# Optimization experiments

Hardware: AMD Instinct MI355X
Metric: run time of the kernel (lower is better)

The kernel has to match this reference:

```python
import jax, jax.numpy as jnp
import numpy as np

B, T, TR, D, H = 8, 1024, 256, 1024, 16
HS = D // H  # head size = 64
FF = 4 * D


def _ln(x, g, b, eps=1e-5):
    m = jnp.mean(x, axis=-1, keepdims=True)
    v = jnp.mean((x - m) ** 2, axis=-1, keepdims=True)
    return (x - m) * jax.lax.rsqrt(v + eps) * g + b


def setup_inputs() -> dict:
    key = jax.random.key(0)
    ks = jax.random.split(key, 24)
    w = lambda i, shape: jax.random.normal(ks[i], shape, dtype=jnp.float32) * 0.02
    return {
        "x": jax.random.normal(ks[0], (B, T, D), dtype=jnp.float32),
        # reduced positional embedding table (gathered by arange == table itself)
        "pos_emb": w(1, (TR, D)),
        # inner standard Block params
        "blk_ln1_g": jnp.ones((D,), jnp.float32), "blk_ln1_b": jnp.zeros((D,), jnp.float32),
        "blk_wq": w(2, (H, D, HS)), "blk_wk": w(3, (H, D, HS)), "blk_wv": w(4, (H, D, HS)),
        "blk_wo": w(5, (D, D)), "blk_bo": jnp.zeros((D,), jnp.float32),
        "blk_ln2_g": jnp.ones((D,), jnp.float32), "blk_ln2_b": jnp.zeros((D,), jnp.float32),
        "blk_w1": w(6, (D, FF)), "blk_b1": jnp.zeros((FF,), jnp.float32),
        "blk_w2": w(7, (FF, D)), "blk_b2": jnp.zeros((D,), jnp.float32),
        # compressing cross-attention params
        "ln1_g": jnp.ones((D,), jnp.float32), "ln1_b": jnp.zeros((D,), jnp.float32),
        "ca_wq": w(8, (H, D, HS)), "ca_wk": w(9, (H, D, HS)), "ca_wv": w(10, (H, D, HS)),
        "ca_wo": w(11, (D, D)), "ca_bo": jnp.zeros((D,), jnp.float32),
        "ln2_g": jnp.ones((D,), jnp.float32), "ln2_b": jnp.zeros((D,), jnp.float32),
        "ff_w1": w(12, (D, FF)), "ff_b1": jnp.zeros((FF,), jnp.float32),
        "ff_w2": w(13, (FF, D)), "ff_b2": jnp.zeros((D,), jnp.float32),
    }


def reference(x, pos_emb, blk_ln1_g, blk_ln1_b, blk_wq, blk_wk, blk_wv, blk_wo, blk_bo,
              blk_ln2_g, blk_ln2_b, blk_w1, blk_b1, blk_w2, blk_b2,
              ln1_g, ln1_b, ca_wq, ca_wk, ca_wv, ca_wo, ca_bo,
              ln2_g, ln2_b, ff_w1, ff_b1, ff_w2, ff_b2):
    b, t, c = x.shape
    scale = c ** -0.5  # matches q @ k^T * c**-0.5 in source

    # ---- inner standard Block: y = x + sa(ln1(x)); y = y + ffwd(ln2(y)) ----
    h = _ln(x, blk_ln1_g, blk_ln1_b)
    q = jnp.einsum('btc,hcs->bhts', h, blk_wq)
    k = jnp.einsum('btc,hcs->bhts', h, blk_wk)
    v = jnp.einsum('btc,hcs->bhts', h, blk_wv)
    wei = jnp.einsum('bhts,bhus->bhtu', q, k) * scale
    causal = jnp.tril(jnp.ones((t, t), dtype=bool))
    wei = jax.nn.softmax(jnp.where(causal, wei, -jnp.inf), axis=-1)
    att = jnp.einsum('bhtu,bhus->bhts', wei, v)
    att = att.transpose(0, 2, 1, 3).reshape(b, t, c) @ blk_wo + blk_bo
    y = x + att
    h2 = _ln(y, blk_ln2_g, blk_ln2_b)
    y = y + (jax.nn.relu(h2 @ blk_w1 + blk_b1) @ blk_w2 + blk_b2)

    # outer residual in CompressingBlock.forward
    x = x + y

    # ---- compressing cross-attention: queries/values from x, keys from pos emb ----
    h1 = _ln(x, ln1_g, ln1_b)
    q = jnp.einsum('btc,hcs->bhts', h1, ca_wq)
    kk = jnp.einsum('rc,hcs->hrs', pos_emb, ca_wk)  # same for every batch
    v = jnp.einsum('btc,hcs->bhts', h1, ca_wv)
    wei = jnp.einsum('bhts,hrs->bhtr', q, kk) * scale  # [b,h,t,tr]
    tr = pos_emb.shape[0]
    mask = jnp.tril(jnp.ones((t, tr), dtype=bool))  # tril[:t,:tr]
    wei = jax.nn.softmax(jnp.where(mask, wei, -jnp.inf), axis=-1)
    # transpose then wei^T @ v -> compressed sequence length tr
    out = jnp.einsum('bhtr,bhts->bhrs', wei, v)
    out = out.transpose(0, 2, 1, 3).reshape(b, tr, c) @ ca_wo + ca_bo

    # ---- final FFN with residual ----
    h3 = _ln(out, ln2_g, ln2_b)
    out = out + (jax.nn.relu(h3 @ ff_w1 + ff_b1) @ ff_w2 + ff_b2)
    return out
```

## Files before the change

kernel.cpp:

```cpp
#include <hip/hip_runtime.h>
#include <stdint.h>

typedef unsigned short u16;
typedef __attribute__((ext_vector_type(8))) short short8;
typedef __attribute__((ext_vector_type(4))) float f32x4;

#define MFMA16(A,B,C) __builtin_amdgcn_mfma_f32_16x16x32_bf16(A,B,C,0,0,0)

static __device__ __forceinline__ u16 f2bf(float f) {
  union { float f; unsigned u; } v; v.f = f;
  unsigned r = v.u + 0x7FFFu + ((v.u >> 16) & 1u);
  return (u16)(r >> 16);
}

static __device__ __forceinline__ void gload16(const void* g, void* l) {
  __builtin_amdgcn_global_load_lds(
      (const __attribute__((address_space(1))) void*)(uintptr_t)g,
      (__attribute__((address_space(3))) void*)(uint32_t)(uintptr_t)l,
      16, 0, 0);
}

static __device__ __forceinline__ int xcd_swz() {
  const int gx = gridDim.x, gy = gridDim.y, nwg = gx * gy;
  const int orig = blockIdx.y * gx + blockIdx.x;
  const int q = nwg >> 3, rm = nwg & 7, xcd = orig & 7, idx = orig >> 3;
  return (xcd < rm ? xcd * (q + 1) : rm * (q + 1) + (xcd - rm) * q) + idx;
}

#define PHASEP(BUFO, KH, STAGE_STMT, TAIL_STMT) do { \
  short8 af_[4], bf_[4]; \
  _Pragma("unroll") \
  for (int mf = 0; mf < 4; ++mf) { \
    const int r = wm0 + mf * 16 + colL; \
    af_[mf] = *(const short8*)&lds[(BUFO) + ((KH) << 12) + r * 32 + ((kgr ^ ((r >> 1) & 3)) << 3)]; \
  } \
  _Pragma("unroll") \
  for (int nf = 0; nf < 4; ++nf) { \
    const int r = wn0 + nf * 16 + colL; \
    bf_[nf] = *(const short8*)&lds[(BUFO) + 8192 + ((KH) << 12) + r * 32 + ((kgr ^ ((r >> 1) & 3)) << 3)]; \
  } \
  STAGE_STMT; \
  __builtin_amdgcn_s_barrier(); \
  asm volatile("s_waitcnt lgkmcnt(0)" ::: "memory"); \
  __builtin_amdgcn_sched_barrier(0); \
  __builtin_amdgcn_s_setprio(1); \
  _Pragma("unroll") \
  for (int mf = 0; mf < 4; ++mf) \
    _Pragma("unroll") \
    for (int nf = 0; nf < 4; ++nf) \
      acc[mf][nf] = MFMA16(af_[mf], bf_[nf], acc[mf][nf]); \
  __builtin_amdgcn_s_setprio(0); \
  __builtin_amdgcn_sched_barrier(0); \
  TAIL_STMT; \
  __builtin_amdgcn_s_barrier(); \
} while (0)

__global__ __launch_bounds__(256) void gemm128p(
    const u16* __restrict__ A, const u16* __restrict__ Wt,
    float* __restrict__ Cf, u16* __restrict__ Cb,
    const float* __restrict__ bias,
    const float* __restrict__ res1, const float* __restrict__ res2,
    int M, int N, int K, int relu)
{
  __shared__ u16 lds[32768];
  const int tid = threadIdx.x;
  const int wid = tid >> 6, lane = tid & 63;
  const int colL = lane & 15, kgr = lane >> 4;
  const int wm0 = (wid & 1) * 64, wn0 = (wid >> 1) * 64;
  const int w = xcd_swz();
  const int m0 = (w / gridDim.y) * 128, n0 = (w % gridDim.y) * 128;
  const int NT = K >> 6;
  f32x4 acc[4][4] = {};

  auto stageP = [&](int t_, int kh) {
    const int kb = t_ * 64 + kh * 32;
    const int baseA = ((t_ & 1) << 14) + (kh << 12);
#pragma unroll
    for (int i = 0; i < 2; ++i) {
      const int c = i * 256 + tid;
      const int row = c >> 2, slot = c & 3;
      const int cs = kb + ((slot ^ ((row >> 1) & 3)) << 3);
      gload16(A  + (size_t)(m0 + row) * K + cs,
              &lds[baseA + ((i * 256 + wid * 64) << 3)]);
      gload16(Wt + (size_t)(n0 + row) * K + cs,
              &lds[baseA + 8192 + ((i * 256 + wid * 64) << 3)]);
    }
  };

  stageP(0, 0); stageP(0, 1); stageP(1, 0);
  asm volatile("s_waitcnt vmcnt(8)" ::: "memory");
  __builtin_amdgcn_s_barrier();

  for (int t = 0; t < NT; ++t) {
    const int bufo = (t & 1) << 14;
    PHASEP(bufo, 0,
           if (t + 1 < NT) stageP(t + 1, 1),
           if (t + 1 < NT) { asm volatile("s_waitcnt vmcnt(8)" ::: "memory"); }
           else            { asm volatile("s_waitcnt vmcnt(0)" ::: "memory"); } );
    PHASEP(bufo, 1,
           if (t + 2 < NT) stageP(t + 2, 0),
           if (t < NT - 2)       { asm volatile("s_waitcnt vmcnt(8)" ::: "memory"); }
           else if (t == NT - 2) { asm volatile("s_waitcnt vmcnt(4)" ::: "memory"); }
           else                  { asm volatile("s_waitcnt vmcnt(0)" ::: "memory"); } );
  }

#pragma unroll
  for (int mf = 0; mf < 4; ++mf) {
#pragma unroll
    for (int nf = 0; nf < 4; ++nf) {
      const int n = n0 + wn0 + nf * 16 + colL;
      const float bv = bias ? bias[n] : 0.f;
#pragma unroll
      for (int rr = 0; rr < 4; ++rr) {
        const int m = m0 + wm0 + mf * 16 + kgr * 4 + rr;
        const size_t off = (size_t)m * N + n;
        float v = acc[mf][nf][rr] + bv;
        if (res1) v += res1[off];
        if (res2) v += res2[off];
        if (relu) v = fmaxf(v, 0.f);
        if (Cf) Cf[off] = v; else Cb[off] = f2bf(v);
      }
    }
  }
}

__global__ __launch_bounds__(256) void ln_rows(
    const float* __restrict__ x, const float* __restrict__ g,
    const float* __restrict__ bt, u16* __restrict__ out)
{
  const int row = blockIdx.x, tid = threadIdx.x;
  const float4 v = ((const float4*)(x + (size_t)row * 1024))[tid];
  float s  = v.x + v.y + v.z + v.w;
  float ss = v.x * v.x + v.y * v.y + v.z * v.z + v.w * v.w;
#pragma unroll
  for (int off = 32; off; off >>= 1) {
    s  += __shfl_xor(s, off);
    ss += __shfl_xor(ss, off);
  }
  __shared__ float red[8];
  const int wid = tid >> 6, lane = tid & 63;
  if (lane == 0) { red[wid] = s; red[4 + wid] = ss; }
  __syncthreads();
  s  = red[0] + red[1] + red[2] + red[3];
  ss = red[4] + red[5] + red[6] + red[7];
  const float mean = s * 0.0009765625f;
  const float var  = ss * 0.0009765625f - mean * mean;
  const float rstd = rsqrtf(var + 1e-5f);
  const float4 gg = ((const float4*)g)[tid];
  const float4 bb = ((const float4*)bt)[tid];
  uint2 ov;
  ov.x = (unsigned)f2bf((v.x - mean) * rstd * gg.x + bb.x) |
         ((unsigned)f2bf((v.y - mean) * rstd * gg.y + bb.y) << 16);
  ov.y = (unsigned)f2bf((v.z - mean) * rstd * gg.z + bb.z) |
         ((unsigned)f2bf((v.w - mean) * rstd * gg.w + bb.w) << 16);
  *(uint2*)(out + (size_t)row * 1024 + tid * 4) = ov;
}

__global__ __launch_bounds__(256) void transpose_w(
    const float* __restrict__ in, u16* __restrict__ out, int R, int C)
{
  __shared__ float t[32][33];
  const int c0 = blockIdx.x * 32, r0 = blockIdx.y * 32;
  const int tx = threadIdx.x & 31, ty = threadIdx.x >> 5;
#pragma unroll
  for (int i = 0; i < 32; i += 8)
    t[ty + i][tx] = in[(size_t)(r0 + ty + i) * C + c0 + tx];
  __syncthreads();
#pragma unroll
  for (int i = 0; i < 32; i += 8)
    out[(size_t)(c0 + ty + i) * R + r0 + tx] = f2bf(t[tx][ty + i]);
}

__global__ __launch_bounds__(256) void pack_head_w(
    const float* __restrict__ w, u16* __restrict__ out)
{
  __shared__ float t[32][33];
  const int h = blockIdx.z;
  const int s0 = blockIdx.x * 32, c0 = blockIdx.y * 32;
  const int tx = threadIdx.x & 31, ty = threadIdx.x >> 5;
#pragma unroll
  for (int i = 0; i < 32; i += 8)
    t[ty + i][tx] = w[((size_t)h * 1024 + c0 + ty + i) * 64 + s0 + tx];
  __syncthreads();
#pragma unroll
  for (int i = 0; i < 32; i += 8)
    out[((size_t)h * 64 + s0 + ty + i) * 1024 + c0 + tx] = f2bf(t[tx][ty + i]);
}

__global__ __launch_bounds__(256) void cvt_bf16(
    const float* __restrict__ in, u16* __restrict__ out)
{
  const int i = blockIdx.x * blockDim.x + threadIdx.x;
  const float4 v = ((const float4*)in)[i];
  uint2 ov;
  ov.x = (unsigned)f2bf(v.x) | ((unsigned)f2bf(v.y) << 16);
  ov.y = (unsigned)f2bf(v.z) | ((unsigned)f2bf(v.w) << 16);
  *(uint2*)(out + (size_t)i * 4) = ov;
}

__global__ __launch_bounds__(256) void vtrans(
    const u16* __restrict__ src, u16* __restrict__ dst, int coloff, int ld)
{
  __shared__ u16 tile[64][65];
  const int t0 = blockIdx.x * 64, h = blockIdx.y, b = blockIdx.z;
  const int lr = threadIdx.x >> 4;
  const int lc = (threadIdx.x & 15) * 4;
#pragma unroll
  for (int i = 0; i < 64; i += 16) {
    const u16* sp = src + (size_t)(b * 1024 + t0 + lr + i) * ld + coloff + h * 64 + lc;
    const uint2 v = *(const uint2*)sp;
    tile[lr + i][lc + 0] = (u16)(v.x & 0xffff);
    tile[lr + i][lc + 1] = (u16)(v.x >> 16);
    tile[lr + i][lc + 2] = (u16)(v.y & 0xffff);
    tile[lr + i][lc + 3] = (u16)(v.y >> 16);
  }
  __syncthreads();
#pragma unroll
  for (int i = 0; i < 64; i += 16) {
    const int s = lr + i;
    uint2 ov;
    ov.x = (unsigned)tile[lc + 0][s] | ((unsigned)tile[lc + 1][s] << 16);
    ov.y = (unsigned)tile[lc + 2][s] | ((unsigned)tile[lc + 3][s] << 16);
    *(uint2*)(dst + (size_t)((b * 16 + h) * 64 + s) * 1024 + t0 + lc) = ov;
  }
}

__global__ __launch_bounds__(512) void attn_inner(
    const u16* __restrict__ qkv, const u16* __restrict__ vt,
    u16* __restrict__ att)
{
  __shared__ u16 Kl[128 * 64];
  __shared__ u16 Vl[64 * 128];
  __shared__ u16 Pl[8 * 16 * 128];
  const int tb = blockIdx.x, h = blockIdx.y, b = blockIdx.z;
  const int tid = threadIdx.x, wid = tid >> 6, lane = tid & 63;
  const int col = lane & 15, kgr = lane >> 4;
  const float scale = 0.03125f;
  short8 qf[2];
  {
    const int trow = tb * 128 + wid * 16 + col;
    const u16* qp = qkv + (size_t)(b * 1024 + trow) * 3072 + h * 64 + kgr * 8;
    qf[0] = *(const short8*)qp;
    qf[1] = *(const short8*)(qp + 32);
  }
  f32x4 o[4] = {};
  float mrun[4], lrun[4];
#pragma unroll
  for (int r = 0; r < 4; ++r) { mrun[r] = -1e30f; lrun[r] = 0.f; }

  for (int kt = 0; kt <= tb * 128; kt += 128) {
#pragma unroll
    for (int i = 0; i < 2; ++i) {
      const int e = i * 4096 + tid * 8;
      const int rk = e >> 6, uk = (e >> 3) & 7;
      gload16(qkv + (size_t)(b * 1024 + kt + rk) * 3072 + 1024 + h * 64 +
                  ((uk ^ (rk & 7)) << 3),
              &Kl[i * 4096 + wid * 512]);
      const int rv = e >> 7, uv = (e >> 3) & 15;
      gload16(vt + (size_t)((b * 16 + h) * 64 + rv) * 1024 + kt +
                  ((uv ^ (rv & 7)) << 3),
              &Vl[i * 4096 + wid * 512]);
    }
    __syncthreads();
    f32x4 s[8];
#pragma unroll
    for (int nt = 0; nt < 8; ++nt) {
      const int rk = nt * 16 + col;
      const short8 k0 = *(const short8*)&Kl[rk * 64 + ((kgr ^ (rk & 7)) << 3)];
      const short8 k1 = *(const short8*)&Kl[rk * 64 + (((kgr + 4) ^ (rk & 7)) << 3)];
      f32x4 a = {};
      a = MFMA16(qf[0], k0, a);
      a = MFMA16(qf[1], k1, a);
      s[nt] = a;
    }
    float mx[4];
#pragma unroll
    for (int r = 0; r < 4; ++r) mx[r] = -1e30f;
    const int tbase = tb * 128 + wid * 16 + kgr * 4;
    if (kt == tb * 128) {
#pragma unroll
      for (int nt = 0; nt < 8; ++nt) {
        const int kp = kt + nt * 16 + col;
#pragma unroll
        for (int r = 0; r < 4; ++r) {
          float v = s[nt][r] * scale;
          if (kp > tbase + r) v = -1e30f;
          s[nt][r] = v;
          mx[r] = fmaxf(mx[r], v);
        }
      }
    } else {
#pragma unroll
      for (int nt = 0; nt < 8; ++nt)
#pragma unroll
        for (int r = 0; r < 4; ++r) {
          const float v = s[nt][r] * scale;
          s[nt][r] = v;
          mx[r] = fmaxf(mx[r], v);
        }
    }
#pragma unroll
    for (int r = 0; r < 4; ++r)
#pragma unroll
      for (int off = 1; off < 16; off <<= 1)
        mx[r] = fmaxf(mx[r], __shfl_xor(mx[r], off));
    float f[4], rs[4];
#pragma unroll
    for (int r = 0; r < 4; ++r) {
      const float mn = fmaxf(mrun[r], mx[r]);
      f[r] = __expf(mrun[r] - mn);
      mrun[r] = mn;
      rs[r] = 0.f;
    }
#pragma unroll
    for (int nt = 0; nt < 8; ++nt)
#pragma unroll
      for (int r = 0; r < 4; ++r) {
        const float p = __expf(s[nt][r] - mrun[r]);
        s[nt][r] = p;
        rs[r] += p;
      }
#pragma unroll
    for (int r = 0; r < 4; ++r) {
#pragma unroll
      for (int off = 1; off < 16; off <<= 1)
        rs[r] += __shfl_xor(rs[r], off);
      lrun[r] = lrun[r] * f[r] + rs[r];
    }
#pragma unroll
    for (int st = 0; st < 4; ++st)
#pragma unroll
      for (int r = 0; r < 4; ++r)
        o[st][r] *= f[r];
    u16* pw = &Pl[wid * 2048];
#pragma unroll
    for (int nt = 0; nt < 8; ++nt)
#pragma unroll
      for (int r = 0; r < 4; ++r) {
        const int rp = kgr * 4 + r;
        pw[rp * 128 + ((nt * 16 + col) ^ ((rp & 7) << 3))] = f2bf(s[nt][r]);
      }
#pragma unroll
    for (int ks = 0; ks < 4; ++ks) {
      const short8 pa = *(const short8*)&pw[col * 128 +
          ((ks * 32 + kgr * 8) ^ ((col & 7) << 3))];
#pragma unroll
      for (int st = 0; st < 4; ++st) {
        const int rv = st * 16 + col;
        const short8 vb = *(const short8*)&Vl[rv * 128 +
            (((ks * 4 + kgr) ^ (rv & 7)) << 3)];
        o[st] = MFMA16(pa, vb, o[st]);
      }
    }
    __syncthreads();
  }
#pragma unroll
  for (int r = 0; r < 4; ++r) {
    const float inv = 1.f / lrun[r];
    const int t = tb * 128 + wid * 16 + kgr * 4 + r;
#pragma unroll
    for (int st = 0; st < 4; ++st)
      att[(size_t)(b * 1024 + t) * 1024 + h * 64 + st * 16 + col] =
          f2bf(o[st][r] * inv);
  }
}

__global__ __launch_bounds__(512) void attn_cross(
    const u16* __restrict__ qv, const u16* __restrict__ kk,
    const u16* __restrict__ vt, u16* __restrict__ outc)
{
  __shared__ u16 KKl[256 * 64];
  __shared__ u16 Vl[64 * 128];
  __shared__ u16 PTl[256 * 128];
  const int h = blockIdx.x, b = blockIdx.y;
  const int tid = threadIdx.x, wid = tid >> 6, lane = tid & 63;
  const int col = lane & 15, kgr = lane >> 4;
  const float scale = 0.03125f;
#pragma unroll
  for (int i = 0; i < 4; ++i) {
    const int e = i * 4096 + tid * 8;
    const int rk = e >> 6, uk = (e >> 3) & 7;
    gload16(kk + (size_t)rk * 1024 + h * 64 + ((uk ^ (rk & 7)) << 3),
            &KKl[i * 4096 + wid * 512]);
  }
  f32x4 oacc[2][4] = {};
  for (int tt = 0; tt < 8; ++tt) {
    const int t0 = tt * 128;
#pragma unroll
    for (int i = 0; i < 2; ++i) {
      const int e = i * 4096 + tid * 8;
      const int rv = e >> 7, uv = (e >> 3) & 15;
      gload16(vt + (size_t)((b * 16 + h) * 64 + rv) * 1024 + t0 +
                  ((uv ^ (rv & 7)) << 3),
              &Vl[i * 4096 + wid * 512]);
    }
    short8 qf0, qf1;
    {
      const int trow = t0 + wid * 16 + col;
      const u16* qp = qv + (size_t)(b * 1024 + trow) * 2048 + h * 64 + kgr * 8;
      qf0 = *(const short8*)qp;
      qf1 = *(const short8*)(qp + 32);
    }
    __syncthreads();
    f32x4 s[16];
#pragma unroll
    for (int rt = 0; rt < 16; ++rt) {
      const int rk = rt * 16 + col;
      const short8 k0 = *(const short8*)&KKl[rk * 64 + ((kgr ^ (rk & 7)) << 3)];
      const short8 k1 = *(const short8*)&KKl[rk * 64 + (((kgr + 4) ^ (rk & 7)) << 3)];
      f32x4 a = {};
      a = MFMA16(qf0, k0, a);
      a = MFMA16(qf1, k1, a);
      s[rt] = a;
    }
    float mx[4];
#pragma unroll
    for (int r = 0; r < 4; ++r) mx[r] = -1e30f;
    const int tbase = t0 + wid * 16 + kgr * 4;
    if (t0 < 256) {
#pragma unroll
      for (int rt = 0; rt < 16; ++rt) {
        const int rp = rt * 16 + col;
#pragma unroll
        for (int r = 0; r < 4; ++r) {
          float v = s[rt][r] * scale;
          if (rp > tbase + r) v = -1e30f;
          s[rt][r] = v;
          mx[r] = fmaxf(mx[r], v);
        }
      }
    } else {
#pragma unroll
      for (int rt = 0; rt < 16; ++rt)
#pragma unroll
        for (int r = 0; r < 4; ++r) {
          const float v = s[rt][r] * scale;
          s[rt][r] = v;
          mx[r] = fmaxf(mx[r], v);
        }
    }
#pragma unroll
    for (int r = 0; r < 4; ++r)
#pragma unroll
      for (int off = 1; off < 16; off <<= 1)
        mx[r] = fmaxf(mx[r], __shfl_xor(mx[r], off));
    float sm[4];
#pragma unroll
    for (int r = 0; r < 4; ++r) sm[r] = 0.f;
#pragma unroll
    for (int rt = 0; rt < 16; ++rt)
#pragma unroll
      for (int r = 0; r < 4; ++r) {
        const float p = __expf(s[rt][r] - mx[r]);
        s[rt][r] = p;
        sm[r] += p;
      }
#pragma unroll
    for (int r = 0; r < 4; ++r) {
#pragma unroll
      for (int off = 1; off < 16; off <<= 1)
        sm[r] += __shfl_xor(sm[r], off);
      sm[r] = 1.f / sm[r];
    }
#pragma unroll
    for (int rt = 0; rt < 16; ++rt)
#pragma unroll
      for (int r = 0; r < 4; ++r) {
        const int rpt = rt * 16 + col;
        PTl[rpt * 128 + ((wid * 16 + kgr * 4 + r) ^ ((rpt & 7) << 3))] =
            f2bf(s[rt][r] * sm[r]);
      }
    __syncthreads();
#pragma unroll
    for (int rr = 0; rr < 2; ++rr) {
      const int rb = (wid * 2 + rr) * 16;
#pragma unroll
      for (int ks = 0; ks < 4; ++ks) {
        const int rpt = rb + col;
        const short8 pa = *(const short8*)&PTl[rpt * 128 +
            ((ks * 32 + kgr * 8) ^ ((rpt & 7) << 3))];
#pragma unroll
        for (int st = 0; st < 4; ++st) {
          const int rv = st * 16 + col;
          const short8 vb = *(const short8*)&Vl[rv * 128 +
              (((ks * 4 + kgr) ^ (rv & 7)) << 3)];
          oacc[rr][st] = MFMA16(pa, vb, oacc[rr][st]);
        }
      }
    }
    __syncthreads();
  }
#pragma unroll
  for (int rr = 0; rr < 2; ++rr)
#pragma unroll
    for (int st = 0; st < 4; ++st)
#pragma unroll
      for (int r = 0; r < 4; ++r) {
        const int rpos = (wid * 2 + rr) * 16 + kgr * 4 + r;
        outc[(size_t)(b * 256 + rpos) * 1024 + h * 64 + st * 16 + col] =
            f2bf(oacc[rr][st][r]);
      }
}

extern "C" void kernel_launch(void* const* d_in, const int* in_sizes, int n_in,
                              void* d_out, int out_size, void* d_ws, size_t ws_size,
                              hipStream_t stream)
{
  const float* x     = (const float*)d_in[0];
  const float* pos   = (const float*)d_in[1];
  const float* bln1g = (const float*)d_in[2];
  const float* bln1b = (const float*)d_in[3];
  const float* bwq   = (const float*)d_in[4];
  const float* bwk   = (const float*)d_in[5];
  const float* bwv   = (const float*)d_in[6];
  const float* bwo   = (const float*)d_in[7];
  const float* bbo   = (const float*)d_in[8];
  const float* bln2g = (const float*)d_in[9];
  const float* bln2b = (const float*)d_in[10];
  const float* bw1   = (const float*)d_in[11];
  const float* bb1   = (const float*)d_in[12];
  const float* bw2   = (const float*)d_in[13];
  const float* bb2   = (const float*)d_in[14];
  const float* ln1g  = (const float*)d_in[15];
  const float* ln1b  = (const float*)d_in[16];
  const float* cwq   = (const float*)d_in[17];
  const float* cwk   = (const float*)d_in[18];
  const float* cwv   = (const float*)d_in[19];
  const float* cwo   = (const float*)d_in[20];
  const float* cbo   = (const float*)d_in[21];
  const float* cln2g = (const float*)d_in[22];
  const float* cln2b = (const float*)d_in[23];
  const float* fw1   = (const float*)d_in[24];
  const float* fb1   = (const float*)d_in[25];
  const float* fw2   = (const float*)d_in[26];
  const float* fb2   = (const float*)d_in[27];

  char* ws = (char*)d_ws;
  size_t off = 0;
  auto alloc = [&](size_t bytes) -> void* {
    void* p = ws + off; off += (bytes + 255) & ~(size_t)255; return p;
  };
  u16* wqkv_t = (u16*)alloc((size_t)3072 * 1024 * 2);
  u16* wo_t   = (u16*)alloc((size_t)1024 * 1024 * 2);
  u16* w1_t   = (u16*)alloc((size_t)4096 * 1024 * 2);
  u16* w2_t   = (u16*)alloc((size_t)1024 * 4096 * 2);
  u16* cwqv_t = (u16*)alloc((size_t)2048 * 1024 * 2);
  u16* cwk_t  = (u16*)alloc((size_t)1024 * 1024 * 2);
  u16* cwo_t  = (u16*)alloc((size_t)1024 * 1024 * 2);
  u16* fw1_t  = (u16*)alloc((size_t)4096 * 1024 * 2);
  u16* fw2_t  = (u16*)alloc((size_t)1024 * 4096 * 2);
  u16* pos_bf = (u16*)alloc((size_t)256 * 1024 * 2);
  u16* kkb    = (u16*)alloc((size_t)256 * 1024 * 2);
  u16* act_ln = (u16*)alloc((size_t)8192 * 1024 * 2);
  u16* qkv    = (u16*)alloc((size_t)8192 * 3072 * 2);
  u16* att    = (u16*)alloc((size_t)8192 * 1024 * 2);
  u16* ffb    = (u16*)alloc((size_t)8192 * 4096 * 2);
  float* yb   = (float*)alloc((size_t)8192 * 1024 * 4);
  if (ws_size < off) return;
  float* x2   = (float*)qkv;
  u16*   qv   = qkv;
  u16*   vt   = ffb;
  u16*   outc = att;
  float* zb   = yb;
  float* outp = (float*)d_out;

  const dim3 B256(256), B512(512);
  pack_head_w<<<dim3(2, 32, 16), B256, 0, stream>>>(bwq, wqkv_t);
  pack_head_w<<<dim3(2, 32, 16), B256, 0, stream>>>(bwk, wqkv_t + 1024 * 1024);
  pack_head_w<<<dim3(2, 32, 16), B256, 0, stream>>>(bwv, wqkv_t + 2048 * 1024);
  transpose_w<<<dim3(32, 32),  B256, 0, stream>>>(bwo, wo_t, 1024, 1024);
  transpose_w<<<dim3(128, 32), B256, 0, stream>>>(bw1, w1_t, 1024, 4096);
  transpose_w<<<dim3(32, 128), B256, 0, stream>>>(bw2, w2_t, 4096, 1024);
  pack_head_w<<<dim3(2, 32, 16), B256, 0, stream>>>(cwq, cwqv_t);
  pack_head_w<<<dim3(2, 32, 16), B256, 0, stream>>>(cwv, cwqv_t + 1024 * 1024);
  pack_head_w<<<dim3(2, 32, 16), B256, 0, stream>>>(cwk, cwk_t);
  transpose_w<<<dim3(32, 32),  B256, 0, stream>>>(cwo, cwo_t, 1024, 1024);
  transpose_w<<<dim3(128, 32), B256, 0, stream>>>(fw1, fw1_t, 1024, 4096);
  transpose_w<<<dim3(32, 128), B256, 0, stream>>>(fw2, fw2_t, 4096, 1024);
  cvt_bf16<<<dim3(256), B256, 0, stream>>>(pos, pos_bf);

  ln_rows<<<dim3(8192), B256, 0, stream>>>(x, bln1g, bln1b, act_ln);
  gemm128p<<<dim3(64, 24), B256, 0, stream>>>(act_ln, wqkv_t, nullptr, qkv,
      nullptr, nullptr, nullptr, 8192, 3072, 1024, 0);
  vtrans<<<dim3(16, 16, 8), B256, 0, stream>>>(qkv, vt, 2048, 3072);
  attn_inner<<<dim3(8, 16, 8), B512, 0, stream>>>(qkv, vt, att);
  gemm128p<<<dim3(64, 8), B256, 0, stream>>>(att, wo_t, yb, nullptr,
      bbo, x, nullptr, 8192, 1024, 1024, 0);
  ln_rows<<<dim3(8192), B256, 0, stream>>>(yb, bln2g, bln2b, act_ln);
  gemm128p<<<dim3(64, 32), B256, 0, stream>>>(act_ln, w1_t, nullptr, ffb,
      bb1, nullptr, nullptr, 8192, 4096, 1024, 1);
  gemm128p<<<dim3(64, 8), B256, 0, stream>>>(ffb, w2_t, x2, nullptr,
      bb2, yb, x, 8192, 1024, 4096, 0);

  ln_rows<<<dim3(8192), B256, 0, stream>>>(x2, ln1g, ln1b, act_ln);
  gemm128p<<<dim3(64, 16), B256, 0, stream>>>(act_ln, cwqv_t, nullptr, qv,
      nullptr, nullptr, nullptr, 8192, 2048, 1024, 0);
  gemm128p<<<dim3(2, 8), B256, 0, stream>>>(pos_bf, cwk_t, nullptr, kkb,
      nullptr, nullptr, nullptr, 256, 1024, 1024, 0);
  vtrans<<<dim3(16, 16, 8), B256, 0, stream>>>(qv, vt, 1024, 2048);
  attn_cross<<<dim3(16, 8), B512, 0, stream>>>(qv, kkb, vt, outc);
  gemm128p<<<dim3(16, 8), B256, 0, stream>>>(outc, cwo_t, zb, nullptr,
      cbo, nullptr, nullptr, 2048, 1024, 1024, 0);

  ln_rows<<<dim3(2048), B256, 0, stream>>>(zb, cln2g, cln2b, act_ln);
  gemm128p<<<dim3(16, 32), B256, 0, stream>>>(act_ln, fw1_t, nullptr, ffb,
      fb1, nullptr, nullptr, 2048, 4096, 1024, 1);
  gemm128p<<<dim3(16, 8), B256, 0, stream>>>(ffb, fw2_t, outp, nullptr,
      fb2, zb, nullptr, 2048, 1024, 4096, 0);
}
```

Before: 753.0 us.

## Pair causal query tiles per attention block and simplify GEMM phase barriers

The inner causal attention kernel now gives each block two query tiles (p and 7-p), so every block does the same amount of work and the K/V tiles loaded into LDS are shared by both query tiles. The grid is halved and the kernel gets an occupancy hint through launch bounds. The GEMM phase macro also drops its mid-phase barrier, lgkmcnt wait, sched_barrier and setprio calls. That lets the compiler schedule LDS reads and MFMAs freely, but removing the explicit wait and barrier could change how the overlap behaves. Register pressure rises because each wave now holds two sets of accumulators.

```diff
diff --git a/kernel.cpp b/kernel.cpp
--- a/kernel.cpp
+++ b/kernel.cpp
@@ -40,19 +40,14 @@
     bf_[nf] = *(const short8*)&lds[(BUFO) + 8192 + ((KH) << 12) + r * 32 + ((kgr ^ ((r >> 1) & 3)) << 3)]; \
   } \
   STAGE_STMT; \
-  __builtin_amdgcn_s_barrier(); \
-  asm volatile("s_waitcnt lgkmcnt(0)" ::: "memory"); \
-  __builtin_amdgcn_sched_barrier(0); \
-  __builtin_amdgcn_s_setprio(1); \
   _Pragma("unroll") \
   for (int mf = 0; mf < 4; ++mf) \
     _Pragma("unroll") \
     for (int nf = 0; nf < 4; ++nf) \
       acc[mf][nf] = MFMA16(af_[mf], bf_[nf], acc[mf][nf]); \
-  __builtin_amdgcn_s_setprio(0); \
-  __builtin_amdgcn_sched_barrier(0); \
   TAIL_STMT; \
   __builtin_amdgcn_s_barrier(); \
+  asm volatile("" ::: "memory"); \
 } while (0)
 
 __global__ __launch_bounds__(256) void gemm128p(
@@ -90,6 +85,7 @@
   stageP(0, 0); stageP(0, 1); stageP(1, 0);
   asm volatile("s_waitcnt vmcnt(8)" ::: "memory");
   __builtin_amdgcn_s_barrier();
+  asm volatile("" ::: "memory");
 
   for (int t = 0; t < NT; ++t) {
     const int bufo = (t & 1) << 14;
@@ -225,30 +221,126 @@
   }
 }
 
-__global__ __launch_bounds__(512) void attn_inner(
+__global__ __launch_bounds__(512, 4) void attn_inner(
     const u16* __restrict__ qkv, const u16* __restrict__ vt,
     u16* __restrict__ att)
 {
   __shared__ u16 Kl[128 * 64];
   __shared__ u16 Vl[64 * 128];
   __shared__ u16 Pl[8 * 16 * 128];
-  const int tb = blockIdx.x, h = blockIdx.y, b = blockIdx.z;
+  const int p = blockIdx.x, h = blockIdx.y, b = blockIdx.z;
+  const int qa = p, qb = 7 - p;
   const int tid = threadIdx.x, wid = tid >> 6, lane = tid & 63;
   const int col = lane & 15, kgr = lane >> 4;
   const float scale = 0.03125f;
-  short8 qf[2];
+  u16* pw = &Pl[wid * 2048];
+
+  short8 qfA[2], qfB[2];
   {
-    const int trow = tb * 128 + wid * 16 + col;
-    const u16* qp = qkv + (size_t)(b * 1024 + trow) * 3072 + h * 64 + kgr * 8;
-    qf[0] = *(const short8*)qp;
-    qf[1] = *(const short8*)(qp + 32);
-  }
-  f32x4 o[4] = {};
-  float mrun[4], lrun[4];
-#pragma unroll
-  for (int r = 0; r < 4; ++r) { mrun[r] = -1e30f; lrun[r] = 0.f; }
-
-  for (int kt = 0; kt <= tb * 128; kt += 128) {
+    const u16* qpA = qkv + (size_t)(b * 1024 + qa * 128 + wid * 16 + col) * 3072 + h * 64 + kgr * 8;
+    qfA[0] = *(const short8*)qpA;  qfA[1] = *(const short8*)(qpA + 32);
+    const u16* qpB = qkv + (size_t)(b * 1024 + qb * 128 + wid * 16 + col) * 3072 + h * 64 + kgr * 8;
+    qfB[0] = *(const short8*)qpB;  qfB[1] = *(const short8*)(qpB + 32);
+  }
+  f32x4 oA[4] = {}, oB[4] = {};
+  float mrA[4], lrA[4], mrB[4], lrB[4];
+#pragma unroll
+  for (int r = 0; r < 4; ++r) { mrA[r] = mrB[r] = -1e30f; lrA[r] = lrB[r] = 0.f; }
+
+  auto do_tile = [&](const short8* qf, f32x4* o, float* mrun, float* lrun,
+                     int tbase, bool diag, int kt) {
+    f32x4 s[8];
+#pragma unroll
+    for (int nt = 0; nt < 8; ++nt) {
+      const int rk = nt * 16 + col;
+      const short8 k0 = *(const short8*)&Kl[rk * 64 + ((kgr ^ (rk & 7)) << 3)];
+      const short8 k1 = *(const short8*)&Kl[rk * 64 + (((kgr + 4) ^ (rk & 7)) << 3)];
+      f32x4 a = {};
+      a = MFMA16(qf[0], k0, a);
+      a = MFMA16(qf[1], k1, a);
+      s[nt] = a;
+    }
+    float mx[4];
+#pragma unroll
+    for (int r = 0; r < 4; ++r) mx[r] = -1e30f;
+    if (diag) {
+#pragma unroll
+      for (int nt = 0; nt < 8; ++nt) {
+        const int kp = kt + nt * 16 + col;
+#pragma unroll
+        for (int r = 0; r < 4; ++r) {
+          float v = s[nt][r] * scale;
+          if (kp > tbase + r) v = -1e30f;
+          s[nt][r] = v;
+          mx[r] = fmaxf(mx[r], v);
+        }
+      }
+    } else {
+#pragma unroll
+      for (int nt = 0; nt < 8; ++nt)
+#pragma unroll
+        for (int r = 0; r < 4; ++r) {
+          const float v = s[nt][r] * scale;
+          s[nt][r] = v;
+          mx[r] = fmaxf(mx[r], v);
+        }
+    }
+#pragma unroll
+    for (int r = 0; r < 4; ++r)
+#pragma unroll
+      for (int off = 1; off < 16; off <<= 1)
+        mx[r] = fmaxf(mx[r], __shfl_xor(mx[r], off));
+    float f[4], rs[4];
+#pragma unroll
+    for (int r = 0; r < 4; ++r) {
+      const float mn = fmaxf(mrun[r], mx[r]);
+      f[r] = __expf(mrun[r] - mn);
+      mrun[r] = mn;
+      rs[r] = 0.f;
+    }
+#pragma unroll
+    for (int nt = 0; nt < 8; ++nt)
+#pragma unroll
+      for (int r = 0; r < 4; ++r) {
+        const float pv = __expf(s[nt][r] - mrun[r]);
+        s[nt][r] = pv;
+        rs[r] += pv;
+      }
+#pragma unroll
+    for (int r = 0; r < 4; ++r) {
+#pragma unroll
+      for (int off = 1; off < 16; off <<= 1)
+        rs[r] += __shfl_xor(rs[r], off);
+      lrun[r] = lrun[r] * f[r] + rs[r];
+    }
+#pragma unroll
+    for (int st = 0; st < 4; ++st)
+#pragma unroll
+      for (int r = 0; r < 4; ++r)
+        o[st][r] *= f[r];
+#pragma unroll
+    for (int nt = 0; nt < 8; ++nt)
+#pragma unroll
+      for (int r = 0; r < 4; ++r) {
+        const int rp = kgr * 4 + r;
+        pw[rp * 128 + ((nt * 16 + col) ^ ((rp & 7) << 3))] = f2bf(s[nt][r]);
+      }
+#pragma unroll
+    for (int ks = 0; ks < 4; ++ks) {
+      const short8 pa = *(const short8*)&pw[col * 128 +
+          ((ks * 32 + kgr * 8) ^ ((col & 7) << 3))];
+#pragma unroll
+      for (int st = 0; st < 4; ++st) {
+        const int rv = st * 16 + col;
+        const short8 vb = *(const short8*)&Vl[rv * 128 +
+            (((ks * 4 + kgr) ^ (rv & 7)) << 3)];
+        o[st] = MFMA16(pa, vb, o[st]);
+      }
+    }
+  };
+
+  for (int ki = 0; ki <= qb; ++ki) {
+    const int kt = ki * 128;
 #pragma unroll
     for (int i = 0; i < 2; ++i) {
       const int e = i * 4096 + tid * 8;
@@ -262,106 +354,23 @@
               &Vl[i * 4096 + wid * 512]);
     }
     __syncthreads();
-    f32x4 s[8];
-#pragma unroll
-    for (int nt = 0; nt < 8; ++nt) {
-      const int rk = nt * 16 + col;
-      const short8 k0 = *(const short8*)&Kl[rk * 64 + ((kgr ^ (rk & 7)) << 3)];
-      const short8 k1 = *(const short8*)&Kl[rk * 64 + (((kgr + 4) ^ (rk & 7)) << 3)];
-      f32x4 a = {};
-      a = MFMA16(qf[0], k0, a);
-      a = MFMA16(qf[1], k1, a);
-      s[nt] = a;
-    }
-    float mx[4];
-#pragma unroll
-    for (int r = 0; r < 4; ++r) mx[r] = -1e30f;
-    const int tbase = tb * 128 + wid * 16 + kgr * 4;
-    if (kt == tb * 128) {
-#pragma unroll
-      for (int nt = 0; nt < 8; ++nt) {
-        const int kp = kt + nt * 16 + col;
-#pragma unroll
-        for (int r = 0; r < 4; ++r) {
-          float v = s[nt][r] * scale;
-          if (kp > tbase + r) v = -1e30f;
-          s[nt][r] = v;
-          mx[r] = fmaxf(mx[r], v);
-        }
-      }
-    } else {
-#pragma unroll
-      for (int nt = 0; nt < 8; ++nt)
-#pragma unroll
-        for (int r = 0; r < 4; ++r) {
-          const float v = s[nt][r] * scale;
-          s[nt][r] = v;
-          mx[r] = fmaxf(mx[r], v);
-        }
-    }
-#pragma unroll
-    for (int r = 0; r < 4; ++r)
-#pragma unroll
-      for (int off = 1; off < 16; off <<= 1)
-        mx[r] = fmaxf(mx[r], __shfl_xor(mx[r], off));
-    float f[4], rs[4];
-#pragma unroll
-    for (int r = 0; r < 4; ++r) {
-      const float mn = fmaxf(mrun[r], mx[r]);
-      f[r] = __expf(mrun[r] - mn);
-      mrun[r] = mn;
-      rs[r] = 0.f;
-    }
-#pragma unroll
-    for (int nt = 0; nt < 8; ++nt)
-#pragma unroll
-      for (int r = 0; r < 4; ++r) {
-        const float p = __expf(s[nt][r] - mrun[r]);
-        s[nt][r] = p;
-        rs[r] += p;
-      }
-#pragma unroll
-    for (int r = 0; r < 4; ++r) {
-#pragma unroll
-      for (int off = 1; off < 16; off <<= 1)
-        rs[r] += __shfl_xor(rs[r], off);
-      lrun[r] = lrun[r] * f[r] + rs[r];
-    }
-#pragma unroll
-    for (int st = 0; st < 4; ++st)
-#pragma unroll
-      for (int r = 0; r < 4; ++r)
-        o[st][r] *= f[r];
-    u16* pw = &Pl[wid * 2048];
-#pragma unroll
-    for (int nt = 0; nt < 8; ++nt)
-#pragma unroll
-      for (int r = 0; r < 4; ++r) {
-        const int rp = kgr * 4 + r;
-        pw[rp * 128 + ((nt * 16 + col) ^ ((rp & 7) << 3))] = f2bf(s[nt][r]);
-      }
-#pragma unroll
-    for (int ks = 0; ks < 4; ++ks) {
-      const short8 pa = *(const short8*)&pw[col * 128 +
-          ((ks * 32 + kgr * 8) ^ ((col & 7) << 3))];
-#pragma unroll
-      for (int st = 0; st < 4; ++st) {
-        const int rv = st * 16 + col;
-        const short8 vb = *(const short8*)&Vl[rv * 128 +
-            (((ks * 4 + kgr) ^ (rv & 7)) << 3)];
-        o[st] = MFMA16(pa, vb, o[st]);
-      }
-    }
+    do_tile(qfB, oB, mrB, lrB, qb * 128 + wid * 16 + kgr * 4, ki == qb, kt);
+    if (ki <= qa)
+      do_tile(qfA, oA, mrA, lrA, qa * 128 + wid * 16 + kgr * 4, ki == qa, kt);
     __syncthreads();
   }
 #pragma unroll
   for (int r = 0; r < 4; ++r) {
-    const float inv = 1.f / lrun[r];
-    const int t = tb * 128 + wid * 16 + kgr * 4 + r;
-#pragma unroll
-    for (int st = 0; st < 4; ++st)
-      att[(size_t)(b * 1024 + t) * 1024 + h * 64 + st * 16 + col] =
-          f2bf(o[st][r] * inv);
+    const float invA = 1.f / lrA[r], invB = 1.f / lrB[r];
+    const int tA = qa * 128 + wid * 16 + kgr * 4 + r;
+    const int tB = qb * 128 + wid * 16 + kgr * 4 + r;
+#pragma unroll
+    for (int st = 0; st < 4; ++st) {
+      att[(size_t)(b * 1024 + tA) * 1024 + h * 64 + st * 16 + col] =
+          f2bf(oA[st][r] * invA);
+      att[(size_t)(b * 1024 + tB) * 1024 + h * 64 + st * 16 + col] =
+          f2bf(oB[st][r] * invB);
+    }
   }
 }
 
@@ -451,9 +460,9 @@
     for (int rt = 0; rt < 16; ++rt)
 #pragma unroll
       for (int r = 0; r < 4; ++r) {
-        const float p = __expf(s[rt][r] - mx[r]);
-        s[rt][r] = p;
-        sm[r] += p;
+        const float pv = __expf(s[rt][r] - mx[r]);
+        s[rt][r] = pv;
+        sm[r] += pv;
       }
 #pragma unroll
     for (int r = 0; r < 4; ++r) {
@@ -583,7 +592,7 @@
   gemm128p<<<dim3(64, 24), B256, 0, stream>>>(act_ln, wqkv_t, nullptr, qkv,
       nullptr, nullptr, nullptr, 8192, 3072, 1024, 0);
   vtrans<<<dim3(16, 16, 8), B256, 0, stream>>>(qkv, vt, 2048, 3072);
-  attn_inner<<<dim3(8, 16, 8), B512, 0, stream>>>(qkv, vt, att);
+  attn_inner<<<dim3(4, 16, 8), B512, 0, stream>>>(qkv, vt, att);
   gemm128p<<<dim3(64, 8), B256, 0, stream>>>(att, wo_t, yb, nullptr,
       bbo, x, nullptr, 8192, 1024, 1024, 0);
   ln_rows<<<dim3(8192), B256, 0, stream>>>(yb, bln2g, bln2b, act_ln);
```

Result: slower. 1.015 ms (+34.7%).
